# Performance work log

Hardware: AMD Instinct MI355X
Metric: run time of the kernel (lower is better)

Reference implementation:

```python
import jax, jax.numpy as jnp
import numpy as np

B, N, C_IN, H, C_OUT = 8, 1024, 256, 4, 256
C = C_OUT // H  # per-head dim = 64
ALPHA = 0.2
NEG_INF = -9e15


def setup_inputs() -> dict:
    key = jax.random.key(0)
    k1, k2, k3, k4, k5 = jax.random.split(key, 5)
    node_feats = jax.random.normal(k1, (B, N, C_IN), dtype=jnp.float32)
    adj_matrix = jax.random.randint(k2, (B, N, N), 0, 2, dtype=jnp.int32)
    # include self-loops as GAT expects
    eye = jnp.eye(N, dtype=jnp.int32)[None]
    adj_matrix = jnp.maximum(adj_matrix, eye)
    # xavier_uniform with gain=1.414
    def xavier(k, shape, fan_in, fan_out, gain=1.414):
        lim = gain * np.sqrt(6.0 / (fan_in + fan_out))
        return jax.random.uniform(k, shape, jnp.float32, -lim, lim)
    W = xavier(k3, (C_OUT, C_IN), C_IN, C_OUT)          # projection weight [out,in]
    b = jnp.zeros((C_OUT,), dtype=jnp.float32)           # projection bias
    a = xavier(k4, (H, 2 * C), 2 * C, H)                 # attention vector per head
    return {"node_feats": node_feats, "adj_matrix": adj_matrix, "W": W, "b": b, "a": a}


def reference(node_feats, adj_matrix, W, b, a):
    Bb, Nn, _ = node_feats.shape
    Hh, twoC = a.shape
    Cc = twoC // 2
    # linear projection -> [B, N, H, C]
    h = (node_feats @ W.T + b).reshape(Bb, Nn, Hh, Cc)
    # edge logit(i,j) = leakyrelu(a . [h_i, h_j]) = leakyrelu(a1.h_i + a2.h_j)
    a_src, a_dst = a[:, :Cc], a[:, Cc:]
    l_src = jnp.einsum('bihc,hc->bih', h, a_src)  # [B,N,H]
    l_dst = jnp.einsum('bjhc,hc->bjh', h, a_dst)  # [B,N,H]
    logits = jax.nn.leaky_relu(l_src[:, :, None, :] + l_dst[:, None, :, :], ALPHA)  # [B,N,N,H]
    logits = jnp.where(adj_matrix[..., None] == 1, logits, NEG_INF)
    probs = jax.nn.softmax(logits, axis=2)  # softmax over neighbors j
    out = jnp.einsum('bijh,bjhc->bihc', probs, h)  # aggregate
    return out.reshape(Bb, Nn, Hh * Cc)  # concat heads
```

## Files before the change

### kernel.cpp

```cpp
#include <hip/hip_runtime.h>
#include <hip/hip_bf16.h>

#define BN   8
#define NN   1024
#define CIN  256
#define COUT 256
#define HH   4
#define CC   64
#define ALPHA_C 0.2f

typedef __attribute__((ext_vector_type(8))) short short8;
typedef __attribute__((ext_vector_type(4))) float f32x4;

__device__ __forceinline__ unsigned short f2bf(float x) {
    __hip_bfloat16 h = __float2bfloat16(x);
    return *(unsigned short*)&h;
}
__device__ __forceinline__ float bf2f(unsigned short u) {
    return __uint_as_float(((unsigned int)u) << 16);
}
__device__ __forceinline__ void gl_lds16(const void* g, void* l) {
    __builtin_amdgcn_global_load_lds(
        (const __attribute__((address_space(1))) void*)g,
        (__attribute__((address_space(3))) void*)l, 16, 0, 0);
}

__global__ __launch_bounds__(256) void k0_wpack(
    const float* __restrict__ W, unsigned short* __restrict__ Whp, unsigned short* __restrict__ Wlp)
{
    const int bid = blockIdx.x;
    const int n = threadIdx.x;
    const int fi = n * 64 + (bid >> 2) * 8 + (bid & 3) * 2;
    const float4* W4 = (const float4*)W;
    float4 wa = W4[fi], wb = W4[fi + 1];
    float xs[8] = {wa.x, wa.y, wa.z, wa.w, wb.x, wb.y, wb.z, wb.w};
    unsigned short hh[8], ll[8];
    #pragma unroll
    for (int e = 0; e < 8; ++e) {
        hh[e] = f2bf(xs[e]);
        ll[e] = f2bf(xs[e] - bf2f(hh[e]));
    }
    *(uint4*)(Whp + ((size_t)bid * 256 + n) * 8) = *(uint4*)hh;
    *(uint4*)(Wlp + ((size_t)bid * 256 + n) * 8) = *(uint4*)ll;
}

__global__ __launch_bounds__(256) void ka_adjpack(
    const int* __restrict__ adj, unsigned int* __restrict__ bmG)
{
    const int bid = blockIdx.x;
    const int b  = bid & 7;
    const int rl = bid >> 3;
    const int wv = threadIdx.x >> 6;
    const int l  = threadIdx.x & 63;
    const int row = b * NN + rl * 4 + wv;
    const int* arow = adj + (size_t)row * NN;
    #pragma unroll 4
    for (int it = 0; it < 16; ++it) {
        int av = arow[it * 64 + l];
        unsigned long long mb = __ballot(av != 0);
        if (l == 0) {
            bmG[row * 32 + 2 * it    ] = (unsigned int)mb;
            bmG[row * 32 + 2 * it + 1] = (unsigned int)(mb >> 32);
        }
    }
}

__global__ __launch_bounds__(1024, 1) void k1_gemm(
    const float* __restrict__ X, const float* __restrict__ bias, const float* __restrict__ a,
    const unsigned short* __restrict__ Whp, const unsigned short* __restrict__ Wlp,
    unsigned short* __restrict__ hbf_p, float* __restrict__ lsrc_t, float* __restrict__ ldst_t)
{
    __shared__ __align__(16) unsigned short Xh[32 * 256];
    __shared__ __align__(16) unsigned short Xl[32 * 256];
    __shared__ float lsP[2][8][2][16];

    const int bid = blockIdx.x;
    const int b  = bid & 7;
    const int tj = bid >> 3;
    const int row0 = b * NN + tj * 32;
    const int tid = threadIdx.x;
    const int wv = tid >> 6, l = tid & 63, il = l & 15, jg = l >> 4;
    const int mq = wv >> 3, no = wv & 7;

    {
        const float4* X4 = (const float4*)(X + (size_t)row0 * CIN);
        #pragma unroll
        for (int it = 0; it < 2; ++it) {
            int f = it * 1024 + tid;
            int r = f >> 6, k4 = f & 63;
            float4 x = X4[f];
            unsigned short h0 = f2bf(x.x), h1 = f2bf(x.y), h2 = f2bf(x.z), h3 = f2bf(x.w);
            unsigned short l0 = f2bf(x.x - bf2f(h0)), l1 = f2bf(x.y - bf2f(h1));
            unsigned short l2 = f2bf(x.z - bf2f(h2)), l3 = f2bf(x.w - bf2f(h3));
            unsigned short hs[4] = {h0, h1, h2, h3}, ls[4] = {l0, l1, l2, l3};
            int off = r * 512 + ((k4 * 8) ^ ((r & 7) << 4));
            *(uint2*)((char*)Xh + off) = *(uint2*)hs;
            *(uint2*)((char*)Xl + off) = *(uint2*)ls;
        }
    }
    __syncthreads();

    f32x4 acc0 = {0.f, 0.f, 0.f, 0.f}, acc1 = acc0;
    {
        const int abase = (mq * 16 + il) * 512;
        const int swz = (il & 7) << 4;
        const short8* Wh8 = (const short8*)Whp;
        const short8* Wl8 = (const short8*)Wlp;
        const int nb = no * 32 + il;
        #pragma unroll
        for (int kc = 0; kc < 8; ++kc) {
            const int ab = abase + ((kc * 64 + jg * 16) ^ swz);
            short8 Ah = *(const short8*)((const char*)Xh + ab);
            short8 Al = *(const short8*)((const char*)Xl + ab);
            const int pidx = (kc * 4 + jg) * 256 + nb;
            short8 Bh0 = Wh8[pidx],      Bl0 = Wl8[pidx];
            short8 Bh1 = Wh8[pidx + 16], Bl1 = Wl8[pidx + 16];
            acc0 = __builtin_amdgcn_mfma_f32_16x16x32_bf16(Ah, Bh0, acc0, 0, 0, 0);
            acc1 = __builtin_amdgcn_mfma_f32_16x16x32_bf16(Ah, Bh1, acc1, 0, 0, 0);
            acc0 = __builtin_amdgcn_mfma_f32_16x16x32_bf16(Ah, Bl0, acc0, 0, 0, 0);
            acc1 = __builtin_amdgcn_mfma_f32_16x16x32_bf16(Ah, Bl1, acc1, 0, 0, 0);
            acc0 = __builtin_amdgcn_mfma_f32_16x16x32_bf16(Al, Bh0, acc0, 0, 0, 0);
            acc1 = __builtin_amdgcn_mfma_f32_16x16x32_bf16(Al, Bh1, acc1, 0, 0, 0);
        }
    }

    const int c0 = no * 32 + il, c1 = c0 + 16;
    const float bia0 = bias[c0], bia1 = bias[c1];
    const int hh = no >> 1;
    const int cc0 = c0 & 63, cc1 = c1 & 63;
    const float as0 = a[hh * 128 + cc0],      as1 = a[hh * 128 + cc1];
    const float ad0 = a[hh * 128 + 64 + cc0], ad1 = a[hh * 128 + 64 + cc1];

    float v0[4], v1[4], psrc[4], pdst[4];
    #pragma unroll
    for (int r = 0; r < 4; ++r) {
        v0[r] = acc0[r] + bia0;
        v1[r] = acc1[r] + bia1;
        psrc[r] = v0[r] * as0 + v1[r] * as1;
        pdst[r] = v0[r] * ad0 + v1[r] * ad1;
    }
    #pragma unroll
    for (int off = 8; off >= 1; off >>= 1) {
        #pragma unroll
        for (int r = 0; r < 4; ++r) {
            psrc[r] += __shfl_xor(psrc[r], off);
            pdst[r] += __shfl_xor(pdst[r], off);
        }
    }
    __syncthreads();

    unsigned short* hp = Xh;
    #pragma unroll
    for (int r = 0; r < 4; ++r) {
        int m = mq * 16 + 4 * jg + r;
        int base = (m >> 3) * 128 + (m & 7);
        hp[(c0 >> 6) * 2048 + ((c0 & 63) >> 4) * 512 + base + (c0 & 15) * 8] = f2bf(v0[r]);
        hp[(c1 >> 6) * 2048 + ((c1 & 63) >> 4) * 512 + base + (c1 & 15) * 8] = f2bf(v1[r]);
    }
    if (il == 0) {
        #pragma unroll
        for (int r = 0; r < 4; ++r) {
            lsP[0][no][mq][4 * jg + r] = psrc[r];
            lsP[1][no][mq][4 * jg + r] = pdst[r];
        }
    }
    __syncthreads();

    {
        uint4* dst4 = (uint4*)(hbf_p + (size_t)(b * 32 + tj) * 8192);
        dst4[tid] = ((const uint4*)hp)[tid];
    }
    if (tid < 256) {
        int sd = tid >> 7, rem = tid & 127, h2 = rem >> 5, m = rem & 31;
        float v = lsP[sd][2 * h2][m >> 4][m & 15] + lsP[sd][2 * h2 + 1][m >> 4][m & 15];
        float* dst = sd ? ldst_t : lsrc_t;
        dst[((size_t)b * HH + h2) * NN + tj * 32 + m] = v;
    }
}

__global__ __launch_bounds__(1024, 1) void k2_attn(
    const unsigned short* __restrict__ hbf_p, const unsigned int* __restrict__ bmG,
    const float* __restrict__ lsrc_t, const float* __restrict__ ldst_t,
    float* __restrict__ out)
{
    __shared__ __align__(16) char smem[152576];
    __shared__ float lsumS[8][2][16];

    unsigned short* hS  = (unsigned short*)smem;
    unsigned int*  bmS  = (unsigned int*)(smem + 131072);
    float*        ldstS = (float*)(smem + 147712);

    const int bid = blockIdx.x;
    const int b  = bid & 7;
    const int hc = bid >> 3;
    const int h  = hc & 3;
    const int i0 = (hc >> 2) * 128;
    const int tid = threadIdx.x;
    const int wv = tid >> 6, l = tid & 63, il = l & 15, jg = l >> 4;
    const int rg = wv >> 1, jhalf = wv & 1;

    {
        #pragma unroll
        for (int k = 0; k < 2; ++k) {
            const int tj = wv * 2 + k;
            #pragma unroll
            for (int cs = 0; cs < 4; ++cs) {
                gl_lds16(hbf_p + ((((size_t)(b * 32 + tj)) * 1024 + h * 256 + cs * 64 + l) << 3),
                         hS + (size_t)(tj * 256 + cs * 64 + l) * 8);
            }
        }
    }
    {
        const unsigned int* bsrc = bmG + ((size_t)(b * NN + i0)) * 32;
        #pragma unroll
        for (int k = 0; k < 4; ++k) {
            int idx = k * 1024 + tid;
            int r = idx >> 5, w = idx & 31;
            bmS[w * 130 + r] = bsrc[idx];
        }
    }
    if (tid < 256)
        ((float4*)ldstS)[tid] = ((const float4*)(ldst_t + ((size_t)(b * HH + h)) * NN))[tid];

    const float lsv = lsrc_t[((size_t)(b * HH + h)) * NN + i0 + rg * 16 + il];

    __syncthreads();

    float mx = -3.4e38f;
    #pragma unroll
    for (int jt = 0; jt < 16; ++jt) mx = fmaxf(mx, ldstS[jt * 64 + l]);
    #pragma unroll
    for (int off = 32; off >= 1; off >>= 1) mx = fmaxf(mx, __shfl_xor(mx, off));
    const float t0  = lsv + mx;
    const float m_r = fmaxf(t0, ALPHA_C * t0);
    float lsum = 0.f;

    f32x4 acc0 = {0.f,0.f,0.f,0.f}, acc1 = acc0, acc2 = acc0, acc3 = acc0;

    const short8* hS8 = (const short8*)hS;

    #pragma unroll 2
    for (int t = 0; t < 16; ++t) {
        const int tj = jhalf * 16 + t;
        short8 c0 = hS8[tj * 256 +   0 + l];
        short8 c1 = hS8[tj * 256 +  64 + l];
        short8 c2 = hS8[tj * 256 + 128 + l];
        short8 c3 = hS8[tj * 256 + 192 + l];
        const unsigned int bw = bmS[tj * 130 + rg * 16 + il] >> (jg * 8);
        const float4 dA = *(const float4*)(ldstS + tj * 32 + jg * 8);
        const float4 dB = *(const float4*)(ldstS + tj * 32 + jg * 8 + 4);

        short8 af;
        #define PELEM(DV, E) {                                   \
            float s_ = lsv + (DV);                               \
            s_ = fmaxf(s_, ALPHA_C * s_);                        \
            float p_ = __expf(s_ - m_r);                         \
            p_ = ((bw >> (E)) & 1u) ? p_ : 0.f;                  \
            lsum += p_;                                          \
            af[E] = (short)f2bf(p_); }
        PELEM(dA.x, 0) PELEM(dA.y, 1) PELEM(dA.z, 2) PELEM(dA.w, 3)
        PELEM(dB.x, 4) PELEM(dB.y, 5) PELEM(dB.z, 6) PELEM(dB.w, 7)
        #undef PELEM

        acc0 = __builtin_amdgcn_mfma_f32_16x16x32_bf16(af, c0, acc0, 0, 0, 0);
        acc1 = __builtin_amdgcn_mfma_f32_16x16x32_bf16(af, c1, acc1, 0, 0, 0);
        acc2 = __builtin_amdgcn_mfma_f32_16x16x32_bf16(af, c2, acc2, 0, 0, 0);
        acc3 = __builtin_amdgcn_mfma_f32_16x16x32_bf16(af, c3, acc3, 0, 0, 0);
    }

    lsum += __shfl_xor(lsum, 16);
    lsum += __shfl_xor(lsum, 32);
    if (l < 16) lsumS[rg][jhalf][il] = lsum;
    __syncthreads();

    float* red = (float*)smem;
    {
        float* rb = red + (rg * 16 + 4 * jg) * 68 + il;
        #define STOREALL(OP) {                                   \
            rb[0 * 68 +  0] OP acc0[0]; rb[0 * 68 + 16] OP acc1[0]; \
            rb[0 * 68 + 32] OP acc2[0]; rb[0 * 68 + 48] OP acc3[0]; \
            rb[1 * 68 +  0] OP acc0[1]; rb[1 * 68 + 16] OP acc1[1]; \
            rb[1 * 68 + 32] OP acc2[1]; rb[1 * 68 + 48] OP acc3[1]; \
            rb[2 * 68 +  0] OP acc0[2]; rb[2 * 68 + 16] OP acc1[2]; \
            rb[2 * 68 + 32] OP acc2[2]; rb[2 * 68 + 48] OP acc3[2]; \
            rb[3 * 68 +  0] OP acc0[3]; rb[3 * 68 + 16] OP acc1[3]; \
            rb[3 * 68 + 32] OP acc2[3]; rb[3 * 68 + 48] OP acc3[3]; }
        if (jhalf == 0) STOREALL(=)
        __syncthreads();
        if (jhalf == 1) STOREALL(+=)
        __syncthreads();
        #undef STOREALL
    }

    #pragma unroll
    for (int pass = 0; pass < 2; ++pass) {
        int row = pass * 64 + (tid >> 4);
        int c4  = tid & 15;
        float4 v = *(const float4*)(red + row * 68 + c4 * 4);
        float ls = lsumS[row >> 4][0][row & 15] + lsumS[row >> 4][1][row & 15];
        float inv = 1.0f / ls;
        float4 o = make_float4(v.x * inv, v.y * inv, v.z * inv, v.w * inv);
        *(float4*)(out + ((size_t)(b * NN + i0 + row)) * COUT + h * 64 + c4 * 4) = o;
    }
}

extern "C" void kernel_launch(void* const* d_in, const int* in_sizes, int n_in,
                              void* d_out, int out_size, void* d_ws, size_t ws_size,
                              hipStream_t stream) {
    const float* X    = (const float*)d_in[0];
    const int*   adj  = (const int*)  d_in[1];
    const float* W    = (const float*)d_in[2];
    const float* bias = (const float*)d_in[3];
    const float* a    = (const float*)d_in[4];
    float* out = (float*)d_out;

    unsigned short* hbf_p = (unsigned short*)d_ws;
    float* lsrc_t = (float*)(hbf_p + (size_t)BN * 32 * 8192);
    float* ldst_t = lsrc_t + (size_t)BN * HH * NN;
    unsigned short* Whp = (unsigned short*)(ldst_t + (size_t)BN * HH * NN);
    unsigned short* Wlp = Whp + 65536;
    unsigned int*   bmG = (unsigned int*)(Wlp + 65536);

    k0_wpack<<<32, 256, 0, stream>>>(W, Whp, Wlp);
    ka_adjpack<<<(BN * NN) / 4, 256, 0, stream>>>(adj, bmG);
    k1_gemm<<<256, 1024, 0, stream>>>(X, bias, a, Whp, Wlp, hbf_p, lsrc_t, ldst_t);
    k2_attn<<<256, 1024, 0, stream>>>(hbf_p, bmG, lsrc_t, ldst_t, out);
}
```

Before: 45.49 us.

## Merge prep kernels and give each attention wave two row tiles over quarter columns

The weight-pack and adjacency-bitmask kernels are merged into a single launch, which removes one kernel launch. In the attention kernel each wave now handles 32 query rows (two 16-row MFMA tiles) across a quarter of the neighbor columns instead of 16 rows across half. Each loaded h fragment is therefore reused for twice as many MFMAs. The cost is more accumulator registers and a four-way partial reduction through two LDS buffers. The bf16 conversion of the probabilities is also changed from round-to-nearest to truncation, which slightly lowers accuracy.

New measurement: 41.51 us (median of 3 runs). 8.8% less time.

```diff
diff --git a/kernel.cpp b/kernel.cpp
--- a/kernel.cpp
+++ b/kernel.cpp
@@ -25,43 +25,43 @@
         (__attribute__((address_space(3))) void*)l, 16, 0, 0);
 }
 
-__global__ __launch_bounds__(256) void k0_wpack(
-    const float* __restrict__ W, unsigned short* __restrict__ Whp, unsigned short* __restrict__ Wlp)
+__global__ __launch_bounds__(256) void kprep(
+    const float* __restrict__ W, const int* __restrict__ adj,
+    unsigned short* __restrict__ Whp, unsigned short* __restrict__ Wlp,
+    unsigned int* __restrict__ bmG)
 {
-    const int bid = blockIdx.x;
-    const int n = threadIdx.x;
-    const int fi = n * 64 + (bid >> 2) * 8 + (bid & 3) * 2;
-    const float4* W4 = (const float4*)W;
-    float4 wa = W4[fi], wb = W4[fi + 1];
-    float xs[8] = {wa.x, wa.y, wa.z, wa.w, wb.x, wb.y, wb.z, wb.w};
-    unsigned short hh[8], ll[8];
-    #pragma unroll
-    for (int e = 0; e < 8; ++e) {
-        hh[e] = f2bf(xs[e]);
-        ll[e] = f2bf(xs[e] - bf2f(hh[e]));
-    }
-    *(uint4*)(Whp + ((size_t)bid * 256 + n) * 8) = *(uint4*)hh;
-    *(uint4*)(Wlp + ((size_t)bid * 256 + n) * 8) = *(uint4*)ll;
-}
-
-__global__ __launch_bounds__(256) void ka_adjpack(
-    const int* __restrict__ adj, unsigned int* __restrict__ bmG)
-{
-    const int bid = blockIdx.x;
-    const int b  = bid & 7;
-    const int rl = bid >> 3;
-    const int wv = threadIdx.x >> 6;
-    const int l  = threadIdx.x & 63;
-    const int row = b * NN + rl * 4 + wv;
-    const int* arow = adj + (size_t)row * NN;
-    #pragma unroll 4
-    for (int it = 0; it < 16; ++it) {
-        int av = arow[it * 64 + l];
-        unsigned long long mb = __ballot(av != 0);
-        if (l == 0) {
-            bmG[row * 32 + 2 * it    ] = (unsigned int)mb;
-            bmG[row * 32 + 2 * it + 1] = (unsigned int)(mb >> 32);
-        }
+    if (blockIdx.x < 2048) {
+        const int bid = blockIdx.x;
+        const int b  = bid & 7;
+        const int rl = bid >> 3;
+        const int wv = threadIdx.x >> 6;
+        const int l  = threadIdx.x & 63;
+        const int row = b * NN + rl * 4 + wv;
+        const int* arow = adj + (size_t)row * NN;
+        #pragma unroll 4
+        for (int it = 0; it < 16; ++it) {
+            int av = arow[it * 64 + l];
+            unsigned long long mb = __ballot(av != 0);
+            if (l == 0) {
+                bmG[row * 32 + 2 * it    ] = (unsigned int)mb;
+                bmG[row * 32 + 2 * it + 1] = (unsigned int)(mb >> 32);
+            }
+        }
+    } else {
+        const int bid = blockIdx.x - 2048;
+        const int n = threadIdx.x;
+        const int fi = n * 64 + (bid >> 2) * 8 + (bid & 3) * 2;
+        const float4* W4 = (const float4*)W;
+        float4 wa = W4[fi], wb = W4[fi + 1];
+        float xs[8] = {wa.x, wa.y, wa.z, wa.w, wb.x, wb.y, wb.z, wb.w};
+        unsigned short hh[8], ll[8];
+        #pragma unroll
+        for (int e = 0; e < 8; ++e) {
+            hh[e] = f2bf(xs[e]);
+            ll[e] = f2bf(xs[e] - bf2f(hh[e]));
+        }
+        *(uint4*)(Whp + ((size_t)bid * 256 + n) * 8) = *(uint4*)hh;
+        *(uint4*)(Wlp + ((size_t)bid * 256 + n) * 8) = *(uint4*)ll;
     }
 }
 
@@ -183,8 +183,8 @@
     const float* __restrict__ lsrc_t, const float* __restrict__ ldst_t,
     float* __restrict__ out)
 {
-    __shared__ __align__(16) char smem[152576];
-    __shared__ float lsumS[8][2][16];
+    __shared__ __align__(16) char smem[151808];
+    __shared__ float lsumS[4][4][32];
 
     unsigned short* hS  = (unsigned short*)smem;
     unsigned int*  bmS  = (unsigned int*)(smem + 131072);
@@ -192,12 +192,11 @@
 
     const int bid = blockIdx.x;
     const int b  = bid & 7;
-    const int hc = bid >> 3;
-    const int h  = hc & 3;
-    const int i0 = (hc >> 2) * 128;
+    const int h  = (bid >> 3) & 3;
+    const int i0 = (bid >> 5) * 128;
     const int tid = threadIdx.x;
     const int wv = tid >> 6, l = tid & 63, il = l & 15, jg = l >> 4;
-    const int rg = wv >> 1, jhalf = wv & 1;
+    const int rg = wv >> 2, jq = wv & 3;
 
     {
         #pragma unroll
@@ -222,7 +221,9 @@
     if (tid < 256)
         ((float4*)ldstS)[tid] = ((const float4*)(ldst_t + ((size_t)(b * HH + h)) * NN))[tid];
 
-    const float lsv = lsrc_t[((size_t)(b * HH + h)) * NN + i0 + rg * 16 + il];
+    const float* lsrc_b = lsrc_t + ((size_t)(b * HH + h)) * NN + i0 + rg * 32;
+    const float lsv0 = lsrc_b[il];
+    const float lsv1 = lsrc_b[16 + il];
 
     __syncthreads();
 
@@ -231,64 +232,93 @@
     for (int jt = 0; jt < 16; ++jt) mx = fmaxf(mx, ldstS[jt * 64 + l]);
     #pragma unroll
     for (int off = 32; off >= 1; off >>= 1) mx = fmaxf(mx, __shfl_xor(mx, off));
-    const float t0  = lsv + mx;
-    const float m_r = fmaxf(t0, ALPHA_C * t0);
-    float lsum = 0.f;
-
-    f32x4 acc0 = {0.f,0.f,0.f,0.f}, acc1 = acc0, acc2 = acc0, acc3 = acc0;
+    float mr0, mr1;
+    { float t_ = lsv0 + mx; mr0 = fmaxf(t_, ALPHA_C * t_); }
+    { float t_ = lsv1 + mx; mr1 = fmaxf(t_, ALPHA_C * t_); }
+    float ls0 = 0.f, ls1 = 0.f;
+
+    f32x4 z4 = {0.f,0.f,0.f,0.f};
+    f32x4 a00 = z4, a01 = z4, a02 = z4, a03 = z4;
+    f32x4 a10 = z4, a11 = z4, a12 = z4, a13 = z4;
 
     const short8* hS8 = (const short8*)hS;
 
     #pragma unroll 2
-    for (int t = 0; t < 16; ++t) {
-        const int tj = jhalf * 16 + t;
+    for (int t = 0; t < 8; ++t) {
+        const int tj = jq * 8 + t;
         short8 c0 = hS8[tj * 256 +   0 + l];
         short8 c1 = hS8[tj * 256 +  64 + l];
         short8 c2 = hS8[tj * 256 + 128 + l];
         short8 c3 = hS8[tj * 256 + 192 + l];
-        const unsigned int bw = bmS[tj * 130 + rg * 16 + il] >> (jg * 8);
+        const unsigned int bw0 = bmS[tj * 130 + rg * 32 + il] >> (jg * 8);
+        const unsigned int bw1 = bmS[tj * 130 + rg * 32 + 16 + il] >> (jg * 8);
         const float4 dA = *(const float4*)(ldstS + tj * 32 + jg * 8);
         const float4 dB = *(const float4*)(ldstS + tj * 32 + jg * 8 + 4);
 
-        short8 af;
-        #define PELEM(DV, E) {                                   \
-            float s_ = lsv + (DV);                               \
+        short8 af0, af1;
+        #define PELEM(AF, E, DV, BWV, LSV, MR, LS) {             \
+            float s_ = (LSV) + (DV);                             \
             s_ = fmaxf(s_, ALPHA_C * s_);                        \
-            float p_ = __expf(s_ - m_r);                         \
-            p_ = ((bw >> (E)) & 1u) ? p_ : 0.f;                  \
-            lsum += p_;                                          \
-            af[E] = (short)f2bf(p_); }
-        PELEM(dA.x, 0) PELEM(dA.y, 1) PELEM(dA.z, 2) PELEM(dA.w, 3)
-        PELEM(dB.x, 4) PELEM(dB.y, 5) PELEM(dB.z, 6) PELEM(dB.w, 7)
+            float p_ = __expf(s_ - (MR));                        \
+            p_ = ((BWV >> (E)) & 1u) ? p_ : 0.f;                 \
+            LS += p_;                                            \
+            AF[E] = (short)(__float_as_uint(p_) >> 16); }
+        PELEM(af0, 0, dA.x, bw0, lsv0, mr0, ls0)
+        PELEM(af0, 1, dA.y, bw0, lsv0, mr0, ls0)
+        PELEM(af0, 2, dA.z, bw0, lsv0, mr0, ls0)
+        PELEM(af0, 3, dA.w, bw0, lsv0, mr0, ls0)
+        PELEM(af0, 4, dB.x, bw0, lsv0, mr0, ls0)
+        PELEM(af0, 5, dB.y, bw0, lsv0, mr0, ls0)
+        PELEM(af0, 6, dB.z, bw0, lsv0, mr0, ls0)
+        PELEM(af0, 7, dB.w, bw0, lsv0, mr0, ls0)
+        PELEM(af1, 0, dA.x, bw1, lsv1, mr1, ls1)
+        PELEM(af1, 1, dA.y, bw1, lsv1, mr1, ls1)
+        PELEM(af1, 2, dA.z, bw1, lsv1, mr1, ls1)
+        PELEM(af1, 3, dA.w, bw1, lsv1, mr1, ls1)
+        PELEM(af1, 4, dB.x, bw1, lsv1, mr1, ls1)
+        PELEM(af1, 5, dB.y, bw1, lsv1, mr1, ls1)
+        PELEM(af1, 6, dB.z, bw1, lsv1, mr1, ls1)
+        PELEM(af1, 7, dB.w, bw1, lsv1, mr1, ls1)
         #undef PELEM
 
-        acc0 = __builtin_amdgcn_mfma_f32_16x16x32_bf16(af, c0, acc0, 0, 0, 0);
-        acc1 = __builtin_amdgcn_mfma_f32_16x16x32_bf16(af, c1, acc1, 0, 0, 0);
-        acc2 = __builtin_amdgcn_mfma_f32_16x16x32_bf16(af, c2, acc2, 0, 0, 0);
-        acc3 = __builtin_amdgcn_mfma_f32_16x16x32_bf16(af, c3, acc3, 0, 0, 0);
-    }
-
-    lsum += __shfl_xor(lsum, 16);
-    lsum += __shfl_xor(lsum, 32);
-    if (l < 16) lsumS[rg][jhalf][il] = lsum;
-    __syncthreads();
-
-    float* red = (float*)smem;
-    {
-        float* rb = red + (rg * 16 + 4 * jg) * 68 + il;
-        #define STOREALL(OP) {                                   \
-            rb[0 * 68 +  0] OP acc0[0]; rb[0 * 68 + 16] OP acc1[0]; \
-            rb[0 * 68 + 32] OP acc2[0]; rb[0 * 68 + 48] OP acc3[0]; \
-            rb[1 * 68 +  0] OP acc0[1]; rb[1 * 68 + 16] OP acc1[1]; \
-            rb[1 * 68 + 32] OP acc2[1]; rb[1 * 68 + 48] OP acc3[1]; \
-            rb[2 * 68 +  0] OP acc0[2]; rb[2 * 68 + 16] OP acc1[2]; \
-            rb[2 * 68 + 32] OP acc2[2]; rb[2 * 68 + 48] OP acc3[2]; \
-            rb[3 * 68 +  0] OP acc0[3]; rb[3 * 68 + 16] OP acc1[3]; \
-            rb[3 * 68 + 32] OP acc2[3]; rb[3 * 68 + 48] OP acc3[3]; }
-        if (jhalf == 0) STOREALL(=)
+        a00 = __builtin_amdgcn_mfma_f32_16x16x32_bf16(af0, c0, a00, 0, 0, 0);
+        a01 = __builtin_amdgcn_mfma_f32_16x16x32_bf16(af0, c1, a01, 0, 0, 0);
+        a02 = __builtin_amdgcn_mfma_f32_16x16x32_bf16(af0, c2, a02, 0, 0, 0);
+        a03 = __builtin_amdgcn_mfma_f32_16x16x32_bf16(af0, c3, a03, 0, 0, 0);
+        a10 = __builtin_amdgcn_mfma_f32_16x16x32_bf16(af1, c0, a10, 0, 0, 0);
+        a11 = __builtin_amdgcn_mfma_f32_16x16x32_bf16(af1, c1, a11, 0, 0, 0);
+        a12 = __builtin_amdgcn_mfma_f32_16x16x32_bf16(af1, c2, a12, 0, 0, 0);
+        a13 = __builtin_amdgcn_mfma_f32_16x16x32_bf16(af1, c3, a13, 0, 0, 0);
+    }
+
+    ls0 += __shfl_xor(ls0, 16); ls0 += __shfl_xor(ls0, 32);
+    ls1 += __shfl_xor(ls1, 16); ls1 += __shfl_xor(ls1, 32);
+    if (l < 16) {
+        lsumS[jq][rg][il] = ls0;
+        lsumS[jq][rg][16 + il] = ls1;
+    }
+    __syncthreads();
+
+    float* red0 = (float*)smem;
+    float* red1 = red0 + 128 * 68;
+    {
+        float* rb = (jq & 1) ? red1 : red0;
+        const int rbase = rg * 32 + 4 * jg;
+        #define STROW(ACC, ROFF, CS, OP) {                                   \
+            rb[(rbase + (ROFF) + 0) * 68 + (CS) * 16 + il] OP ACC[0];        \
+            rb[(rbase + (ROFF) + 1) * 68 + (CS) * 16 + il] OP ACC[1];        \
+            rb[(rbase + (ROFF) + 2) * 68 + (CS) * 16 + il] OP ACC[2];        \
+            rb[(rbase + (ROFF) + 3) * 68 + (CS) * 16 + il] OP ACC[3]; }
+        #define STOREALL(OP) {                                               \
+            STROW(a00, 0, 0, OP) STROW(a01, 0, 1, OP)                        \
+            STROW(a02, 0, 2, OP) STROW(a03, 0, 3, OP)                        \
+            STROW(a10, 16, 0, OP) STROW(a11, 16, 1, OP)                      \
+            STROW(a12, 16, 2, OP) STROW(a13, 16, 3, OP) }
+        if (jq < 2) STOREALL(=)
         __syncthreads();
-        if (jhalf == 1) STOREALL(+=)
+        if (jq >= 2) STOREALL(+=)
         __syncthreads();
+        #undef STROW
         #undef STOREALL
     }
 
@@ -296,10 +326,13 @@
     for (int pass = 0; pass < 2; ++pass) {
         int row = pass * 64 + (tid >> 4);
         int c4  = tid & 15;
-        float4 v = *(const float4*)(red + row * 68 + c4 * 4);
-        float ls = lsumS[row >> 4][0][row & 15] + lsumS[row >> 4][1][row & 15];
+        float4 v0 = *(const float4*)(red0 + row * 68 + c4 * 4);
+        float4 v1 = *(const float4*)(red1 + row * 68 + c4 * 4);
+        float ls = lsumS[0][row >> 5][row & 31] + lsumS[1][row >> 5][row & 31]
+                 + lsumS[2][row >> 5][row & 31] + lsumS[3][row >> 5][row & 31];
         float inv = 1.0f / ls;
-        float4 o = make_float4(v.x * inv, v.y * inv, v.z * inv, v.w * inv);
+        float4 o = make_float4((v0.x + v1.x) * inv, (v0.y + v1.y) * inv,
+                               (v0.z + v1.z) * inv, (v0.w + v1.w) * inv);
         *(float4*)(out + ((size_t)(b * NN + i0 + row)) * COUT + h * 64 + c4 * 4) = o;
     }
 }
@@ -321,8 +354,7 @@
     unsigned short* Wlp = Whp + 65536;
     unsigned int*   bmG = (unsigned int*)(Wlp + 65536);
 
-    k0_wpack<<<32, 256, 0, stream>>>(W, Whp, Wlp);
-    ka_adjpack<<<(BN * NN) / 4, 256, 0, stream>>>(adj, bmG);
+    kprep<<<2048 + 32, 256, 0, stream>>>(W, adj, Whp, Wlp, bmG);
     k1_gemm<<<256, 1024, 0, stream>>>(X, bias, a, Whp, Wlp, hbf_p, lsrc_t, ldst_t);
     k2_attn<<<256, 1024, 0, stream>>>(hbf_p, bmG, lsrc_t, ldst_t, out);
 }
```
